# Performance work log

Hardware: AMD Instinct MI355X
Metric: run time of the kernel (lower is better)

Reference implementation:

```python
import jax, jax.numpy as jnp
import numpy as np

BATCH, SEQ_LEN, D_MODEL, STATE = 4, 2048, 64, 64


def setup_inputs() -> dict:
    key = jax.random.key(0)
    ks = jax.random.split(key, 6)
    def w(k, shape):
        return (jax.random.normal(k, shape, jnp.float32) * 0.05)
    return {
        "x": jax.random.normal(ks[0], (BATCH, SEQ_LEN, D_MODEL), jnp.float32),
        "W1": w(ks[1], (D_MODEL, D_MODEL)),  # fc1: d -> d (delta)
        "b1": jnp.zeros((D_MODEL,), jnp.float32),
        "W2": w(ks[2], (D_MODEL, STATE)),    # fc2: d -> n (B)
        "b2": jnp.zeros((STATE,), jnp.float32),
        "W3": w(ks[3], (D_MODEL, STATE)),    # fc3: d -> n (C)
        "b3": jnp.zeros((STATE,), jnp.float32),
        "A": w(ks[4], (D_MODEL, STATE)),     # A parameter [d, n]
    }


def reference(x, W1, b1, W2, b2, W3, b3, A):
    # x: [b, l, d]
    Bm = x @ W2 + b2                               # [b, l, n]
    C = x @ W3 + b3                                # [b, l, n]
    delta = jax.nn.softplus(x @ W1 + b1)           # [b, l, d]
    # discretization (as in original torch code)
    dA = jnp.exp(jnp.einsum('bld,dn->bldn', delta, A))   # [b, l, d, n]
    dB = delta[..., None] * Bm[:, :, None, :]            # [b, l, d, n]
    # h_prev is zeros in the original forward, so dA * h_prev == 0
    h = dA * 0.0 + x[..., None] * dB                     # [b, l, d, n]
    y = jnp.einsum('bln,bldn->bld', C, h)                # [b, l, d]
    return y
```

## Files before the change

### kernel.cpp

```cpp
#include <hip/hip_runtime.h>
#include <cmath>

#define BATCH 4
#define SEQLEN 2048
#define DMODEL 64
#define NTOK (BATCH * SEQLEN)
#define TOK_PER_WAVE 4
#define WAVES_PER_BLOCK 8
#define TOK_PER_BLOCK (TOK_PER_WAVE * WAVES_PER_BLOCK)
#define NBLOCKS (NTOK / TOK_PER_BLOCK)

__global__ __launch_bounds__(512, 2) void s6_fused_kernel(
    const float* __restrict__ x,
    const float* __restrict__ W1, const float* __restrict__ b1,
    const float* __restrict__ W2, const float* __restrict__ b2,
    const float* __restrict__ W3, const float* __restrict__ b3,
    float* __restrict__ y)
{
    __shared__ float sW[3][DMODEL * DMODEL];

    const int tid = threadIdx.x;
    const int lane = tid & 63;
    const int wave = tid >> 6;

    float4 wreg[3][2];
    {
        const float4* g0 = (const float4*)W1;
        const float4* g1 = (const float4*)W2;
        const float4* g2 = (const float4*)W3;
        #pragma unroll
        for (int i0 = 0; i0 < 2; ++i0) {
            const int i = tid + 512 * i0;
            wreg[0][i0] = g0[i];
            wreg[1][i0] = g1[i];
            wreg[2][i0] = g2[i];
        }
    }

    const int tok0 = __builtin_amdgcn_readfirstlane(
        (blockIdx.x * WAVES_PER_BLOCK + wave) * TOK_PER_WAVE);
    const float* __restrict__ xb = x + (size_t)tok0 * DMODEL;

    float xv[TOK_PER_WAVE];
    #pragma unroll
    for (int t = 0; t < TOK_PER_WAVE; ++t)
        xv[t] = x[(size_t)(tok0 + t) * DMODEL + lane];

    const float bb1 = b1[lane], bb2 = b2[lane], bb3 = b3[lane];

    #pragma unroll
    for (int m = 0; m < 3; ++m) {
        #pragma unroll
        for (int i0 = 0; i0 < 2; ++i0) {
            const int i  = tid + 512 * i0;
            const int k  = i >> 4;
            const int d0 = (i & 15) << 2;
            const int slot = (((k >> 2) ^ (i & 7)) << 2) + (k & 3);
            const float* w = (const float*)&wreg[m][i0];
            float* base = sW[m];
            #pragma unroll
            for (int j = 0; j < 4; ++j)
                base[(d0 + j) * DMODEL + slot] = w[j];
        }
    }

    float a1[TOK_PER_WAVE], a2[TOK_PER_WAVE], a3[TOK_PER_WAVE];
    #pragma unroll
    for (int t = 0; t < TOK_PER_WAVE; ++t) { a1[t] = bb1; a2[t] = bb2; a3[t] = bb3; }

    __syncthreads();

    const int swz = (lane >> 2) & 7;
    const float* __restrict__ r1 = sW[0] + lane * DMODEL;
    const float* __restrict__ r2 = sW[1] + lane * DMODEL;
    const float* __restrict__ r3 = sW[2] + lane * DMODEL;

    #pragma unroll
    for (int kk = 0; kk < DMODEL / 4; ++kk) {
        const int off = (kk ^ swz) << 2;
        const float4 w1 = *(const float4*)(r1 + off);
        const float4 w2 = *(const float4*)(r2 + off);
        const float4 w3 = *(const float4*)(r3 + off);
        #pragma unroll
        for (int t = 0; t < TOK_PER_WAVE; ++t) {
            const float* xr = xb + t * DMODEL + kk * 4;
            const float x0 = xr[0], x1 = xr[1], x2 = xr[2], x3 = xr[3];
            a1[t] = fmaf(x3, w1.w, fmaf(x2, w1.z, fmaf(x1, w1.y, fmaf(x0, w1.x, a1[t]))));
            a2[t] = fmaf(x3, w2.w, fmaf(x2, w2.z, fmaf(x1, w2.y, fmaf(x0, w2.x, a2[t]))));
            a3[t] = fmaf(x3, w3.w, fmaf(x2, w3.z, fmaf(x1, w3.y, fmaf(x0, w3.x, a3[t]))));
        }
    }

    #pragma unroll
    for (int t = 0; t < TOK_PER_WAVE; ++t) {
        const float delta = log1pf(expf(a1[t]));
        float prod = a2[t] * a3[t];
        #pragma unroll
        for (int off = 32; off > 0; off >>= 1)
            prod += __shfl_xor(prod, off);
        y[(size_t)(tok0 + t) * DMODEL + lane] = xv[t] * delta * prod;
    }
}

extern "C" void kernel_launch(void* const* d_in, const int* in_sizes, int n_in,
                              void* d_out, int out_size, void* d_ws, size_t ws_size,
                              hipStream_t stream) {
    const float* x  = (const float*)d_in[0];
    const float* W1 = (const float*)d_in[1];
    const float* b1 = (const float*)d_in[2];
    const float* W2 = (const float*)d_in[3];
    const float* b2 = (const float*)d_in[4];
    const float* W3 = (const float*)d_in[5];
    const float* b3 = (const float*)d_in[6];
    float* y = (float*)d_out;

    s6_fused_kernel<<<NBLOCKS, 512, 0, stream>>>(x, W1, b1, W2, b2, W3, b3, y);
}
```

Baseline: 12.82 us.

## Store weights as bf16 in shared memory and use DPP row-rotate reductions

Weights are rounded to bf16 and packed in pairs into shared memory. This halves LDS footprint and the bytes each lane reads per k-step, using a new swizzle for the packed layout. The cross-lane sum now uses DPP row_ror adds within 16-lane rows and only two shuffles across rows. The bf16 weights add rounding error against the fp32 reference, and the extra unpack ALU work may offset the savings.

```diff
diff --git a/kernel.cpp b/kernel.cpp
--- a/kernel.cpp
+++ b/kernel.cpp
@@ -10,6 +10,20 @@
 #define TOK_PER_BLOCK (TOK_PER_WAVE * WAVES_PER_BLOCK)
 #define NBLOCKS (NTOK / TOK_PER_BLOCK)
 
+__device__ __forceinline__ unsigned f2bf(float f) {
+    unsigned u = __builtin_bit_cast(unsigned, f);
+    return (u + 0x7FFFu + ((u >> 16) & 1u)) >> 16;
+}
+__device__ __forceinline__ float bf_lo(unsigned u) { return __builtin_bit_cast(float, u << 16); }
+__device__ __forceinline__ float bf_hi(unsigned u) { return __builtin_bit_cast(float, u & 0xFFFF0000u); }
+
+template <int CTRL>
+__device__ __forceinline__ float dpp_ror_add(float v) {
+    int x = __builtin_bit_cast(int, v);
+    int y = __builtin_amdgcn_update_dpp(0, x, CTRL, 0xF, 0xF, true);
+    return v + __builtin_bit_cast(float, y);
+}
+
 __global__ __launch_bounds__(512, 2) void s6_fused_kernel(
     const float* __restrict__ x,
     const float* __restrict__ W1, const float* __restrict__ b1,
@@ -17,24 +31,23 @@
     const float* __restrict__ W3, const float* __restrict__ b3,
     float* __restrict__ y)
 {
-    __shared__ float sW[3][DMODEL * DMODEL];
+    __shared__ unsigned sW[3][DMODEL * 32];
 
-    const int tid = threadIdx.x;
+    const int tid  = threadIdx.x;
     const int lane = tid & 63;
     const int wave = tid >> 6;
 
-    float4 wreg[3][2];
+    const int r  = tid >> 4;
+    const int dg = tid & 15;
+    float4 f0[3], f1[3];
     {
         const float4* g0 = (const float4*)W1;
         const float4* g1 = (const float4*)W2;
         const float4* g2 = (const float4*)W3;
-        #pragma unroll
-        for (int i0 = 0; i0 < 2; ++i0) {
-            const int i = tid + 512 * i0;
-            wreg[0][i0] = g0[i];
-            wreg[1][i0] = g1[i];
-            wreg[2][i0] = g2[i];
-        }
+        const int i0 = (2 * r) * 16 + dg, i1 = (2 * r + 1) * 16 + dg;
+        f0[0] = g0[i0]; f1[0] = g0[i1];
+        f0[1] = g1[i0]; f1[1] = g1[i1];
+        f0[2] = g2[i0]; f1[2] = g2[i1];
     }
 
     const int tok0 = __builtin_amdgcn_readfirstlane(
@@ -50,17 +63,13 @@
 
     #pragma unroll
     for (int m = 0; m < 3; ++m) {
+        const float* p0 = (const float*)&f0[m];
+        const float* p1 = (const float*)&f1[m];
         #pragma unroll
-        for (int i0 = 0; i0 < 2; ++i0) {
-            const int i  = tid + 512 * i0;
-            const int k  = i >> 4;
-            const int d0 = (i & 15) << 2;
-            const int slot = (((k >> 2) ^ (i & 7)) << 2) + (k & 3);
-            const float* w = (const float*)&wreg[m][i0];
-            float* base = sW[m];
-            #pragma unroll
-            for (int j = 0; j < 4; ++j)
-                base[(d0 + j) * DMODEL + slot] = w[j];
+        for (int jj = 0; jj < 4; ++jj) {
+            const int d = dg * 4 + jj;
+            const unsigned v = f2bf(p0[jj]) | (f2bf(p1[jj]) << 16);
+            sW[m][d * 32 + 2 * ((r >> 1) ^ (d & 15)) + (r & 1)] = v;
         }
     }
 
@@ -70,24 +79,27 @@
 
     __syncthreads();
 
-    const int swz = (lane >> 2) & 7;
-    const float* __restrict__ r1 = sW[0] + lane * DMODEL;
-    const float* __restrict__ r2 = sW[1] + lane * DMODEL;
-    const float* __restrict__ r3 = sW[2] + lane * DMODEL;
+    const unsigned* __restrict__ r1 = sW[0] + lane * 32;
+    const unsigned* __restrict__ r2 = sW[1] + lane * 32;
+    const unsigned* __restrict__ r3 = sW[2] + lane * 32;
+    const int lsw = lane & 15;
 
     #pragma unroll
     for (int kk = 0; kk < DMODEL / 4; ++kk) {
-        const int off = (kk ^ swz) << 2;
-        const float4 w1 = *(const float4*)(r1 + off);
-        const float4 w2 = *(const float4*)(r2 + off);
-        const float4 w3 = *(const float4*)(r3 + off);
+        const int off = 2 * (kk ^ lsw);
+        const uint2 u1 = *(const uint2*)(r1 + off);
+        const uint2 u2 = *(const uint2*)(r2 + off);
+        const uint2 u3 = *(const uint2*)(r3 + off);
+        const float w10 = bf_lo(u1.x), w11 = bf_hi(u1.x), w12 = bf_lo(u1.y), w13 = bf_hi(u1.y);
+        const float w20 = bf_lo(u2.x), w21 = bf_hi(u2.x), w22 = bf_lo(u2.y), w23 = bf_hi(u2.y);
+        const float w30 = bf_lo(u3.x), w31 = bf_hi(u3.x), w32 = bf_lo(u3.y), w33 = bf_hi(u3.y);
         #pragma unroll
         for (int t = 0; t < TOK_PER_WAVE; ++t) {
             const float* xr = xb + t * DMODEL + kk * 4;
             const float x0 = xr[0], x1 = xr[1], x2 = xr[2], x3 = xr[3];
-            a1[t] = fmaf(x3, w1.w, fmaf(x2, w1.z, fmaf(x1, w1.y, fmaf(x0, w1.x, a1[t]))));
-            a2[t] = fmaf(x3, w2.w, fmaf(x2, w2.z, fmaf(x1, w2.y, fmaf(x0, w2.x, a2[t]))));
-            a3[t] = fmaf(x3, w3.w, fmaf(x2, w3.z, fmaf(x1, w3.y, fmaf(x0, w3.x, a3[t]))));
+            a1[t] = fmaf(x3, w13, fmaf(x2, w12, fmaf(x1, w11, fmaf(x0, w10, a1[t]))));
+            a2[t] = fmaf(x3, w23, fmaf(x2, w22, fmaf(x1, w21, fmaf(x0, w20, a2[t]))));
+            a3[t] = fmaf(x3, w33, fmaf(x2, w32, fmaf(x1, w31, fmaf(x0, w30, a3[t]))));
         }
     }
 
@@ -95,9 +107,12 @@
     for (int t = 0; t < TOK_PER_WAVE; ++t) {
         const float delta = log1pf(expf(a1[t]));
         float prod = a2[t] * a3[t];
-        #pragma unroll
-        for (int off = 32; off > 0; off >>= 1)
-            prod += __shfl_xor(prod, off);
+        prod = dpp_ror_add<0x121>(prod);
+        prod = dpp_ror_add<0x122>(prod);
+        prod = dpp_ror_add<0x124>(prod);
+        prod = dpp_ror_add<0x128>(prod);
+        prod += __shfl_xor(prod, 16);
+        prod += __shfl_xor(prod, 32);
         y[(size_t)(tok0 + t) * DMODEL + lane] = xv[t] * delta * prod;
     }
 }
```

Result: faster. 12.16 us (-5.2%).
